# Kernel optimization log

Hardware: AMD Instinct MI355X
Metric: run time of the kernel (lower is better)

## Reference

```python
import jax, jax.numpy as jnp
import numpy as np
import math

D_MODEL = 1024
NUM_HEADS = 16
D_KEY = D_MODEL // NUM_HEADS  # 64, used only for the softmax scale
B, S = 4, 2048


def setup_inputs() -> dict:
    key = jax.random.key(0)
    ks = jax.random.split(key, 7)
    scale = 1.0 / math.sqrt(D_MODEL)
    x = jax.random.normal(ks[0], (B, S, D_MODEL), dtype=jnp.float32)
    # torch.nn.Linear params: weight [out, in], bias [out]
    Wq = jax.random.normal(ks[1], (D_MODEL, D_MODEL), dtype=jnp.float32) * scale
    bq = jax.random.normal(ks[2], (D_MODEL,), dtype=jnp.float32) * scale
    Wk = jax.random.normal(ks[3], (D_MODEL, D_MODEL), dtype=jnp.float32) * scale
    bk = jax.random.normal(ks[4], (D_MODEL,), dtype=jnp.float32) * scale
    Wv = jax.random.normal(ks[5], (D_MODEL, D_MODEL), dtype=jnp.float32) * scale
    bv = jax.random.normal(ks[6], (D_MODEL,), dtype=jnp.float32) * scale
    return {"x": x, "Wq": Wq, "bq": bq, "Wk": Wk, "bk": bk, "Wv": Wv, "bv": bv}


def reference(x, Wq, bq, Wk, bk, Wv, bv):
    # Q, K, V projections (torch Linear: x @ W.T + b)
    Q = jnp.einsum('bsd,ed->bse', x, Wq) + bq  # [B,S,D]
    K = jnp.einsum('bsd,ed->bse', x, Wk) + bk
    V = jnp.einsum('bsd,ed->bse', x, Wv) + bv
    inv_sqrt_dk = 1.0 / math.sqrt(D_KEY)
    # full-width attention (no head split, as in the source forward)
    scores = jnp.einsum('bqd,bkd->bqk', Q, K) * inv_sqrt_dk  # [B,S,S]
    weights = jax.nn.softmax(scores, axis=-1)
    return jnp.einsum('bqk,bkd->bqd', weights, V)  # [B,S,D]
```

## Files before the change

kernel.cpp:

```cpp
#include <hip/hip_runtime.h>
#include <stdint.h>

#define S_LEN 2048
#define DMODEL 1024
#define NBATCH 4
#define MROWS (NBATCH * S_LEN)

typedef __bf16 bf16x8 __attribute__((ext_vector_type(8)));
typedef float f32x4 __attribute__((ext_vector_type(4)));

__device__ __forceinline__ unsigned short f2bf(float f) {
  unsigned int x = __builtin_bit_cast(unsigned int, f);
  x += 0x7FFFu + ((x >> 16) & 1u);
  return (unsigned short)(x >> 16);
}

template <int N>
__device__ __forceinline__ void waitvm() {
  static_assert(N <= 8, "vmcnt range");
  if constexpr (N < 0) {}
  else if constexpr (N == 0) asm volatile("s_waitcnt vmcnt(0)" ::: "memory");
  else if constexpr (N == 1) asm volatile("s_waitcnt vmcnt(1)" ::: "memory");
  else if constexpr (N == 2) asm volatile("s_waitcnt vmcnt(2)" ::: "memory");
  else if constexpr (N == 3) asm volatile("s_waitcnt vmcnt(3)" ::: "memory");
  else if constexpr (N == 4) asm volatile("s_waitcnt vmcnt(4)" ::: "memory");
  else if constexpr (N == 5) asm volatile("s_waitcnt vmcnt(5)" ::: "memory");
  else if constexpr (N == 6) asm volatile("s_waitcnt vmcnt(6)" ::: "memory");
  else if constexpr (N == 7) asm volatile("s_waitcnt vmcnt(7)" ::: "memory");
  else asm volatile("s_waitcnt vmcnt(8)" ::: "memory");
}
#define BARRIER() do { __builtin_amdgcn_s_barrier(); asm volatile("" ::: "memory"); } while (0)
#define LGKM0() asm volatile("s_waitcnt lgkmcnt(0)" ::: "memory")

__global__ void prep_all_kernel(const float* __restrict__ x, const float* __restrict__ Wq,
                                const float* __restrict__ Wk, const float* __restrict__ Wv,
                                const float* __restrict__ bq, const float* __restrict__ bk,
                                ushort4* __restrict__ xb, ushort4* __restrict__ Wqkb,
                                ushort4* __restrict__ Wvb, float4* __restrict__ bqk) {
  const int NX = MROWS * DMODEL / 4;
  const int NW = DMODEL * DMODEL / 4;
  int i = blockIdx.x * blockDim.x + threadIdx.x;
  float4 v;
  if (i < NX) {
    v = reinterpret_cast<const float4*>(x)[i];
    ushort4 o; o.x = f2bf(v.x); o.y = f2bf(v.y); o.z = f2bf(v.z); o.w = f2bf(v.w);
    xb[i] = o;
  } else {
    int j = i - NX;
    if (j < NW) v = reinterpret_cast<const float4*>(Wq)[j];
    else if (j < 2 * NW) v = reinterpret_cast<const float4*>(Wk)[j - NW];
    else v = reinterpret_cast<const float4*>(Wv)[j - 2 * NW];
    ushort4 o; o.x = f2bf(v.x); o.y = f2bf(v.y); o.z = f2bf(v.z); o.w = f2bf(v.w);
    if (j < 2 * NW) Wqkb[j] = o;
    else Wvb[j - 2 * NW] = o;
    if (j < 512) bqk[j] = (j < 256) ? reinterpret_cast<const float4*>(bq)[j]
                                    : reinterpret_cast<const float4*>(bk)[j - 256];
  }
}

template <int BM_, int EP, int NT>
__global__ __launch_bounds__(512, 2) void gemm8(
    const unsigned short* __restrict__ A, const unsigned short* __restrict__ Bm,
    void* __restrict__ Cp, const float* __restrict__ bias,
    int lda, int ldb, int ldc, float scale,
    long zsA, long zsB, long zsC) {
  constexpr int BN_ = 256;
  constexpr int BK = 64;
  constexpr int RA = BM_ / 128;
  constexpr int HALF_A = (BM_ / 2) * 128;
  constexpr int HALF_B = 128 * 128;
  constexpr int ATILE = BM_ * 128;
  constexpr int BTILE = BN_ * 128;
  constexpr int MREP = BM_ / 32;
  constexpr int MQ = MREP / 2;

  __shared__ alignas(16) char lds[(ATILE + BTILE) * 2];

  const int tid = threadIdx.x;
  const int l = tid & 63;
  const int w = tid >> 6;
  const int wm = w >> 2;
  const int wn = w & 3;

  const int gx = gridDim.x;
  const int nwg = gridDim.x * gridDim.y;
  int n = blockIdx.y * gx + blockIdx.x;
  int n2 = (n & 7) * (nwg >> 3) + (n >> 3);
  const int tileM = (n2 / gx) * BM_;
  const int tileN = (n2 % gx) * BN_;

  const int z = blockIdx.z;
  const unsigned short* Ab = A + (size_t)z * zsA;
  const unsigned short* Bb = Bm + (size_t)z * zsB;

  const int srow = l >> 3;
  const int scol = (((l & 7) ^ srow) * 16);

  auto stageA = [&](int buf, int t, int h) {
#pragma unroll
    for (int r = 0; r < RA; ++r) {
      int row = h * (BM_ / 2) + r * 64 + w * 8 + srow;
      const char* g = (const char*)(Ab + (size_t)(tileM + row) * lda + t * BK) + scol;
      char* d = lds + buf * (ATILE + BTILE) + h * HALF_A + r * 8192 + w * 1024;
      __builtin_amdgcn_global_load_lds(
          (const __attribute__((address_space(1))) void*)g,
          (__attribute__((address_space(3))) void*)d, 16, 0, 0);
    }
  };
  auto stageB = [&](int buf, int t, int h) {
#pragma unroll
    for (int r = 0; r < 2; ++r) {
      int row = h * 128 + r * 64 + w * 8 + srow;
      const char* g = (const char*)(Bb + (size_t)(tileN + row) * ldb + t * BK) + scol;
      char* d = lds + buf * (ATILE + BTILE) + ATILE + h * HALF_B + r * 8192 + w * 1024;
      __builtin_amdgcn_global_load_lds(
          (const __attribute__((address_space(1))) void*)g,
          (__attribute__((address_space(3))) void*)d, 16, 0, 0);
    }
  };

  f32x4 acc[MREP][4];
#pragma unroll
  for (int m = 0; m < MREP; ++m)
#pragma unroll
    for (int nn = 0; nn < 4; ++nn) acc[m][nn] = f32x4{0.f, 0.f, 0.f, 0.f};

  const int frow = l & 15;
  auto rdA = [&](int buf, int mh, int m, int kk) -> bf16x8 {
    int row = mh * (BM_ / 2) + wm * (BM_ / 4) + m * 16 + frow;
    int col = (kk * 64 + ((l >> 4) * 16)) ^ ((row & 7) << 4);
    return *reinterpret_cast<const bf16x8*>(lds + buf * (ATILE + BTILE) + row * 128 + col);
  };
  auto rdB = [&](int buf, int nh, int nn, int kk) -> bf16x8 {
    int row = nh * 128 + wn * 32 + nn * 16 + frow;
    int col = (kk * 64 + ((l >> 4) * 16)) ^ ((row & 7) << 4);
    return *reinterpret_cast<const bf16x8*>(lds + buf * (ATILE + BTILE) + ATILE + row * 128 + col);
  };

  bf16x8 avF[MQ][2];
  bf16x8 bv0[2][2], bv1[2][2];

  auto rdAfull = [&](int buf, int mh) {
#pragma unroll
    for (int m = 0; m < MQ; ++m)
#pragma unroll
      for (int kk = 0; kk < 2; ++kk) avF[m][kk] = rdA(buf, mh, m, kk);
  };
  auto rdBfull = [&](int buf, int nh, bf16x8 (&bv)[2][2]) {
#pragma unroll
    for (int nn = 0; nn < 2; ++nn)
#pragma unroll
      for (int kk = 0; kk < 2; ++kk) bv[nn][kk] = rdB(buf, nh, nn, kk);
  };
  auto mfc = [&](int mh, bf16x8 (&bv)[2][2], int nh) {
    __builtin_amdgcn_s_setprio(1);
#pragma unroll
    for (int kk = 0; kk < 2; ++kk)
#pragma unroll
      for (int m = 0; m < MQ; ++m)
#pragma unroll
        for (int nn = 0; nn < 2; ++nn)
          acc[mh * MQ + m][nh * 2 + nn] = __builtin_amdgcn_mfma_f32_16x16x32_bf16(
              avF[m][kk], bv[nn][kk], acc[mh * MQ + m][nh * 2 + nn], 0, 0, 0);
    __builtin_amdgcn_s_setprio(0);
  };
  auto mfc2 = [&](int mh) {
    __builtin_amdgcn_s_setprio(1);
#pragma unroll
    for (int kk = 0; kk < 2; ++kk)
#pragma unroll
      for (int m = 0; m < MQ; ++m) {
#pragma unroll
        for (int nn = 0; nn < 2; ++nn)
          acc[mh * MQ + m][2 + nn] = __builtin_amdgcn_mfma_f32_16x16x32_bf16(
              avF[m][kk], bv1[nn][kk], acc[mh * MQ + m][2 + nn], 0, 0, 0);
#pragma unroll
        for (int nn = 0; nn < 2; ++nn)
          acc[mh * MQ + m][nn] = __builtin_amdgcn_mfma_f32_16x16x32_bf16(
              avF[m][kk], bv0[nn][kk], acc[mh * MQ + m][nn], 0, 0, 0);
      }
    __builtin_amdgcn_s_setprio(0);
  };

  stageA(0, 0, 0);
  stageB(0, 0, 0);
  stageB(0, 0, 1);
  stageA(0, 0, 1);
  waitvm<0>();
  BARRIER();

#pragma unroll 2
  for (int t = 0; t < NT - 1; ++t) {
    const int buf = t & 1, nb = buf ^ 1;
    rdAfull(buf, 0); rdBfull(buf, 0, bv0);
    stageA(nb, t + 1, 0); stageB(nb, t + 1, 0);
    mfc(0, bv0, 0);
    rdBfull(buf, 1, bv1);
    stageB(nb, t + 1, 1);
    mfc(0, bv1, 1);
    rdAfull(buf, 1);
    stageA(nb, t + 1, 1);
    mfc2(1);
    LGKM0();
    waitvm<0>();
    BARRIER();
  }
  {
    const int buf = (NT - 1) & 1;
    rdAfull(buf, 0); rdBfull(buf, 0, bv0);
    mfc(0, bv0, 0);
    rdBfull(buf, 1, bv1);
    mfc(0, bv1, 1);
    rdAfull(buf, 1);
    mfc2(1);
  }

  const int lr = (l >> 4) * 4;
  const int lc = l & 15;
#pragma unroll
  for (int mh = 0; mh < 2; ++mh) {
#pragma unroll
    for (int m = 0; m < MQ; ++m) {
#pragma unroll
      for (int nh = 0; nh < 2; ++nh) {
#pragma unroll
        for (int nn = 0; nn < 2; ++nn) {
          int gr = tileM + mh * (BM_ / 2) + wm * (BM_ / 4) + m * 16 + lr;
          int gc = tileN + nh * 128 + wn * 32 + nn * 16 + lc;
          f32x4 v = acc[mh * MQ + m][nh * 2 + nn];
          if constexpr (EP == 0 || EP == 3) {
            unsigned short* C = (unsigned short*)Cp + (size_t)z * zsC;
#pragma unroll
            for (int j = 0; j < 4; ++j) {
              float bb = (EP == 0) ? bias[gc] : bias[gr + j];
              C[(size_t)(gr + j) * ldc + gc] = f2bf(v[j] + bb);
            }
          } else {
            float* C = (float*)Cp + (size_t)z * zsC;
#pragma unroll
            for (int j = 0; j < 4; ++j)
              C[(size_t)(gr + j) * ldc + gc] = (EP == 1) ? v[j] * scale : v[j];
          }
        }
      }
    }
  }
}

__global__ __launch_bounds__(256) void softmax_kernel(const float* __restrict__ Sb,
                                                      unsigned short* __restrict__ P) {
  const size_t row = blockIdx.x;
  const float* sp = Sb + row * S_LEN;
  const int t = threadIdx.x;
  const int wid = t >> 6, lane = t & 63;
  float4 v0 = reinterpret_cast<const float4*>(sp)[t * 2];
  float4 v1 = reinterpret_cast<const float4*>(sp)[t * 2 + 1];
  float s[8] = {v0.x, v0.y, v0.z, v0.w, v1.x, v1.y, v1.z, v1.w};
  float mx = s[0];
#pragma unroll
  for (int i = 1; i < 8; ++i) mx = fmaxf(mx, s[i]);
#pragma unroll
  for (int o = 32; o > 0; o >>= 1) mx = fmaxf(mx, __shfl_xor(mx, o));
  __shared__ float redm[4];
  __shared__ float reds[4];
  if (lane == 0) redm[wid] = mx;
  __syncthreads();
  mx = fmaxf(fmaxf(redm[0], redm[1]), fmaxf(redm[2], redm[3]));
  float e[8];
  float sum = 0.f;
#pragma unroll
  for (int i = 0; i < 8; ++i) { e[i] = __expf(s[i] - mx); sum += e[i]; }
#pragma unroll
  for (int o = 32; o > 0; o >>= 1) sum += __shfl_xor(sum, o);
  if (lane == 0) reds[wid] = sum;
  __syncthreads();
  sum = reds[0] + reds[1] + reds[2] + reds[3];
  float inv = 1.0f / sum;
  ushort4 o0, o1;
  o0.x = f2bf(e[0] * inv); o0.y = f2bf(e[1] * inv); o0.z = f2bf(e[2] * inv); o0.w = f2bf(e[3] * inv);
  o1.x = f2bf(e[4] * inv); o1.y = f2bf(e[5] * inv); o1.z = f2bf(e[6] * inv); o1.w = f2bf(e[7] * inv);
  ushort4* dp = reinterpret_cast<ushort4*>(P + row * S_LEN);
  dp[t * 2] = o0;
  dp[t * 2 + 1] = o1;
}

extern "C" void kernel_launch(void* const* d_in, const int* in_sizes, int n_in,
                              void* d_out, int out_size, void* d_ws, size_t ws_size,
                              hipStream_t stream) {
  (void)in_sizes; (void)n_in; (void)out_size;
  const float* x = (const float*)d_in[0];
  const float* Wq = (const float*)d_in[1];
  const float* bq = (const float*)d_in[2];
  const float* Wk = (const float*)d_in[3];
  const float* bk = (const float*)d_in[4];
  const float* Wv = (const float*)d_in[5];
  const float* bv = (const float*)d_in[6];
  float* out = (float*)d_out;

  if (ws_size < 141557760ull) return;
  char* ws = (char*)d_ws;
  unsigned short* xb   = (unsigned short*)(ws);
  unsigned short* Wqkb = (unsigned short*)(ws + 16777216);
  unsigned short* Wvb  = (unsigned short*)(ws + 20971520);
  float*          bqk  = (float*)(ws + 23068672);
  unsigned short* QKb  = (unsigned short*)(ws + 24117248);
  float*          Sb   = (float*)(ws + 57671680);
  unsigned short* Vt   = (unsigned short*)(ws + 124780544);
  unsigned short* P    = QKb;

  const int NX = MROWS * DMODEL / 4, NW = DMODEL * DMODEL / 4;
  prep_all_kernel<<<dim3((NX + 3 * NW) / 256), 256, 0, stream>>>(
      x, Wq, Wk, Wv, bq, bk, (ushort4*)xb, (ushort4*)Wqkb, (ushort4*)Wvb, (float4*)bqk);

  gemm8<256, 0, 16><<<dim3(8, 32, 1), 512, 0, stream>>>(
      xb, Wqkb, QKb, bqk, 1024, 1024, 2048, 1.f, 0, 0, 0);

  gemm8<128, 3, 16><<<dim3(8, 8, 4), 512, 0, stream>>>(
      Wvb, xb, Vt, bv, 1024, 1024, 2048, 1.f,
      0, (long)S_LEN * DMODEL, (long)DMODEL * S_LEN);

  gemm8<256, 1, 16><<<dim3(8, 8, 4), 512, 0, stream>>>(
      QKb, QKb + 1024, Sb, nullptr, 2048, 2048, 2048, 0.125f,
      (long)S_LEN * 2048, (long)S_LEN * 2048, (long)S_LEN * S_LEN);

  softmax_kernel<<<dim3(MROWS), 256, 0, stream>>>(Sb, P);

  gemm8<128, 2, 32><<<dim3(4, 16, 4), 512, 0, stream>>>(
      P, Vt, out, nullptr, 2048, 2048, 1024, 1.f,
      (long)S_LEN * S_LEN, (long)DMODEL * S_LEN, (long)S_LEN * DMODEL);
}
```

Measured before the change: 169.2 us.

## Switch GEMM to triple-buffered LDS pipeline with fixed 128-row tiles

The GEMM kernel now uses three LDS buffers and prefetches two k-tiles ahead, waiting with a partial vmcnt instead of draining all loads each iteration. This is meant to hide global-to-LDS latency behind the MFMA work. The M tile is fixed at 128 rows for all GEMMs, so the QK projection and score GEMMs launch twice as many workgroups with smaller tiles. The change uses more LDS per block (3x48KB), which may limit occupancy at two blocks per CU, and lowers data reuse for the GEMMs that previously used 256-row tiles.

```diff
diff --git a/kernel.cpp b/kernel.cpp
--- a/kernel.cpp
+++ b/kernel.cpp
@@ -58,23 +58,23 @@
   }
 }
 
-template <int BM_, int EP, int NT>
+template <int EP, int NT>
 __global__ __launch_bounds__(512, 2) void gemm8(
     const unsigned short* __restrict__ A, const unsigned short* __restrict__ Bm,
     void* __restrict__ Cp, const float* __restrict__ bias,
     int lda, int ldb, int ldc, float scale,
     long zsA, long zsB, long zsC) {
+  constexpr int BM_ = 128;
   constexpr int BN_ = 256;
   constexpr int BK = 64;
-  constexpr int RA = BM_ / 128;
-  constexpr int HALF_A = (BM_ / 2) * 128;
+  constexpr int HALF_A = 64 * 128;
   constexpr int HALF_B = 128 * 128;
   constexpr int ATILE = BM_ * 128;
   constexpr int BTILE = BN_ * 128;
-  constexpr int MREP = BM_ / 32;
-  constexpr int MQ = MREP / 2;
-
-  __shared__ alignas(16) char lds[(ATILE + BTILE) * 2];
+  constexpr int BUF = ATILE + BTILE;
+  constexpr int MQ = 2;
+
+  __shared__ alignas(16) char lds[BUF * 3];
 
   const int tid = threadIdx.x;
   const int l = tid & 63;
@@ -97,44 +97,47 @@
   const int scol = (((l & 7) ^ srow) * 16);
 
   auto stageA = [&](int buf, int t, int h) {
-#pragma unroll
-    for (int r = 0; r < RA; ++r) {
-      int row = h * (BM_ / 2) + r * 64 + w * 8 + srow;
-      const char* g = (const char*)(Ab + (size_t)(tileM + row) * lda + t * BK) + scol;
-      char* d = lds + buf * (ATILE + BTILE) + h * HALF_A + r * 8192 + w * 1024;
+    int row = h * 64 + w * 8 + srow;
+    const char* g = (const char*)(Ab + (size_t)(tileM + row) * lda + t * BK) + scol;
+    char* d = lds + buf * BUF + h * HALF_A + w * 1024;
+    __builtin_amdgcn_global_load_lds(
+        (const __attribute__((address_space(1))) void*)g,
+        (__attribute__((address_space(3))) void*)d, 16, 0, 0);
+  };
+  auto stageB = [&](int buf, int t, int h) {
+#pragma unroll
+    for (int r = 0; r < 2; ++r) {
+      int row = h * 128 + r * 64 + w * 8 + srow;
+      const char* g = (const char*)(Bb + (size_t)(tileN + row) * ldb + t * BK) + scol;
+      char* d = lds + buf * BUF + ATILE + h * HALF_B + r * 8192 + w * 1024;
       __builtin_amdgcn_global_load_lds(
           (const __attribute__((address_space(1))) void*)g,
           (__attribute__((address_space(3))) void*)d, 16, 0, 0);
     }
   };
-  auto stageB = [&](int buf, int t, int h) {
-#pragma unroll
-    for (int r = 0; r < 2; ++r) {
-      int row = h * 128 + r * 64 + w * 8 + srow;
-      const char* g = (const char*)(Bb + (size_t)(tileN + row) * ldb + t * BK) + scol;
-      char* d = lds + buf * (ATILE + BTILE) + ATILE + h * HALF_B + r * 8192 + w * 1024;
-      __builtin_amdgcn_global_load_lds(
-          (const __attribute__((address_space(1))) void*)g,
-          (__attribute__((address_space(3))) void*)d, 16, 0, 0);
-    }
-  };
-
-  f32x4 acc[MREP][4];
-#pragma unroll
-  for (int m = 0; m < MREP; ++m)
+  auto stageT = [&](int buf, int t) {
+    stageA(buf, t, 0);
+    stageB(buf, t, 0);
+    stageB(buf, t, 1);
+    stageA(buf, t, 1);
+  };
+
+  f32x4 acc[4][4];
+#pragma unroll
+  for (int m = 0; m < 4; ++m)
 #pragma unroll
     for (int nn = 0; nn < 4; ++nn) acc[m][nn] = f32x4{0.f, 0.f, 0.f, 0.f};
 
   const int frow = l & 15;
   auto rdA = [&](int buf, int mh, int m, int kk) -> bf16x8 {
-    int row = mh * (BM_ / 2) + wm * (BM_ / 4) + m * 16 + frow;
+    int row = mh * 64 + wm * 32 + m * 16 + frow;
     int col = (kk * 64 + ((l >> 4) * 16)) ^ ((row & 7) << 4);
-    return *reinterpret_cast<const bf16x8*>(lds + buf * (ATILE + BTILE) + row * 128 + col);
+    return *reinterpret_cast<const bf16x8*>(lds + buf * BUF + row * 128 + col);
   };
   auto rdB = [&](int buf, int nh, int nn, int kk) -> bf16x8 {
     int row = nh * 128 + wn * 32 + nn * 16 + frow;
     int col = (kk * 64 + ((l >> 4) * 16)) ^ ((row & 7) << 4);
-    return *reinterpret_cast<const bf16x8*>(lds + buf * (ATILE + BTILE) + ATILE + row * 128 + col);
+    return *reinterpret_cast<const bf16x8*>(lds + buf * BUF + ATILE + row * 128 + col);
   };
 
   bf16x8 avF[MQ][2];
@@ -182,37 +185,37 @@
     __builtin_amdgcn_s_setprio(0);
   };
 
-  stageA(0, 0, 0);
-  stageB(0, 0, 0);
-  stageB(0, 0, 1);
-  stageA(0, 0, 1);
-  waitvm<0>();
-  BARRIER();
-
-#pragma unroll 2
-  for (int t = 0; t < NT - 1; ++t) {
-    const int buf = t & 1, nb = buf ^ 1;
-    rdAfull(buf, 0); rdBfull(buf, 0, bv0);
-    stageA(nb, t + 1, 0); stageB(nb, t + 1, 0);
-    mfc(0, bv0, 0);
-    rdBfull(buf, 1, bv1);
-    stageB(nb, t + 1, 1);
-    mfc(0, bv1, 1);
-    rdAfull(buf, 1);
-    stageA(nb, t + 1, 1);
-    mfc2(1);
-    LGKM0();
-    waitvm<0>();
-    BARRIER();
-  }
-  {
-    const int buf = (NT - 1) & 1;
+  auto tile_reads_mfma = [&](int buf) {
     rdAfull(buf, 0); rdBfull(buf, 0, bv0);
     mfc(0, bv0, 0);
     rdBfull(buf, 1, bv1);
     mfc(0, bv1, 1);
     rdAfull(buf, 1);
     mfc2(1);
+  };
+
+  stageT(0, 0);
+  stageT(1, 1);
+  waitvm<6>();
+  BARRIER();
+
+#pragma unroll 3
+  for (int t = 0; t < NT - 2; ++t) {
+    const int buf = t % 3;
+    stageT((t + 2) % 3, t + 2);
+    tile_reads_mfma(buf);
+    LGKM0();
+    waitvm<6>();
+    BARRIER();
+  }
+  {
+    tile_reads_mfma((NT - 2) % 3);
+    LGKM0();
+    waitvm<0>();
+    BARRIER();
+  }
+  {
+    tile_reads_mfma((NT - 1) % 3);
   }
 
   const int lr = (l >> 4) * 4;
@@ -225,7 +228,7 @@
       for (int nh = 0; nh < 2; ++nh) {
 #pragma unroll
         for (int nn = 0; nn < 2; ++nn) {
-          int gr = tileM + mh * (BM_ / 2) + wm * (BM_ / 4) + m * 16 + lr;
+          int gr = tileM + mh * 64 + wm * 32 + m * 16 + lr;
           int gc = tileN + nh * 128 + wn * 32 + nn * 16 + lc;
           f32x4 v = acc[mh * MQ + m][nh * 2 + nn];
           if constexpr (EP == 0 || EP == 3) {
@@ -312,20 +315,20 @@
   prep_all_kernel<<<dim3((NX + 3 * NW) / 256), 256, 0, stream>>>(
       x, Wq, Wk, Wv, bq, bk, (ushort4*)xb, (ushort4*)Wqkb, (ushort4*)Wvb, (float4*)bqk);
 
-  gemm8<256, 0, 16><<<dim3(8, 32, 1), 512, 0, stream>>>(
+  gemm8<0, 16><<<dim3(8, 64, 1), 512, 0, stream>>>(
       xb, Wqkb, QKb, bqk, 1024, 1024, 2048, 1.f, 0, 0, 0);
 
-  gemm8<128, 3, 16><<<dim3(8, 8, 4), 512, 0, stream>>>(
+  gemm8<3, 16><<<dim3(8, 8, 4), 512, 0, stream>>>(
       Wvb, xb, Vt, bv, 1024, 1024, 2048, 1.f,
       0, (long)S_LEN * DMODEL, (long)DMODEL * S_LEN);
 
-  gemm8<256, 1, 16><<<dim3(8, 8, 4), 512, 0, stream>>>(
+  gemm8<1, 16><<<dim3(8, 16, 4), 512, 0, stream>>>(
       QKb, QKb + 1024, Sb, nullptr, 2048, 2048, 2048, 0.125f,
       (long)S_LEN * 2048, (long)S_LEN * 2048, (long)S_LEN * S_LEN);
 
   softmax_kernel<<<dim3(MROWS), 256, 0, stream>>>(Sb, P);
 
-  gemm8<128, 2, 32><<<dim3(4, 16, 4), 512, 0, stream>>>(
+  gemm8<2, 32><<<dim3(4, 16, 4), 512, 0, stream>>>(
       P, Vt, out, nullptr, 2048, 2048, 1024, 1.f,
       (long)S_LEN * S_LEN, (long)DMODEL * S_LEN, (long)S_LEN * DMODEL);
 }
```

After: 178.9 us. 5.8% more time.

## Restructure GEMM main loop into barrier-separated phases with finer-grained prefetch staging

Applied to the files above, without the earlier changes.

Rewrites the double-buffered GEMM mainloop so the global-to-LDS prefetch for tile t+2 is split into quarter-tile pieces issued between MFMA phases. Each phase is fenced by barriers and explicit lgkm/vmcnt waits, which allows partial vmcnt waits instead of draining all loads each iteration. The prologue preloads nearly two stages and the last two iterations are peeled. This is meant to overlap memory traffic with MFMA work more evenly, at the cost of many extra workgroup barriers and sched_barrier fences that constrain the compiler's scheduling.

```diff
diff --git a/kernel.cpp b/kernel.cpp
--- a/kernel.cpp
+++ b/kernel.cpp
@@ -30,7 +30,8 @@
   else asm volatile("s_waitcnt vmcnt(8)" ::: "memory");
 }
 #define BARRIER() do { __builtin_amdgcn_s_barrier(); asm volatile("" ::: "memory"); } while (0)
-#define LGKM0() asm volatile("s_waitcnt lgkmcnt(0)" ::: "memory")
+#define LGKM0() do { asm volatile("s_waitcnt lgkmcnt(0)" ::: "memory"); \
+                     __builtin_amdgcn_sched_barrier(0); } while (0)
 
 __global__ void prep_all_kernel(const float* __restrict__ x, const float* __restrict__ Wq,
                                 const float* __restrict__ Wk, const float* __restrict__ Wv,
@@ -71,10 +72,11 @@
   constexpr int HALF_B = 128 * 128;
   constexpr int ATILE = BM_ * 128;
   constexpr int BTILE = BN_ * 128;
-  constexpr int MREP = BM_ / 32;
-  constexpr int MQ = MREP / 2;
-
-  __shared__ alignas(16) char lds[(ATILE + BTILE) * 2];
+  constexpr int BUF = ATILE + BTILE;
+  constexpr int MQ = BM_ / 64;
+  constexpr int VM = (BM_ == 256) ? 6 : 4;
+
+  __shared__ alignas(16) char lds[BUF * 2];
 
   const int tid = threadIdx.x;
   const int l = tid & 63;
@@ -101,7 +103,7 @@
     for (int r = 0; r < RA; ++r) {
       int row = h * (BM_ / 2) + r * 64 + w * 8 + srow;
       const char* g = (const char*)(Ab + (size_t)(tileM + row) * lda + t * BK) + scol;
-      char* d = lds + buf * (ATILE + BTILE) + h * HALF_A + r * 8192 + w * 1024;
+      char* d = lds + buf * BUF + h * HALF_A + r * 8192 + w * 1024;
       __builtin_amdgcn_global_load_lds(
           (const __attribute__((address_space(1))) void*)g,
           (__attribute__((address_space(3))) void*)d, 16, 0, 0);
@@ -112,16 +114,16 @@
     for (int r = 0; r < 2; ++r) {
       int row = h * 128 + r * 64 + w * 8 + srow;
       const char* g = (const char*)(Bb + (size_t)(tileN + row) * ldb + t * BK) + scol;
-      char* d = lds + buf * (ATILE + BTILE) + ATILE + h * HALF_B + r * 8192 + w * 1024;
+      char* d = lds + buf * BUF + ATILE + h * HALF_B + r * 8192 + w * 1024;
       __builtin_amdgcn_global_load_lds(
           (const __attribute__((address_space(1))) void*)g,
           (__attribute__((address_space(3))) void*)d, 16, 0, 0);
     }
   };
 
-  f32x4 acc[MREP][4];
-#pragma unroll
-  for (int m = 0; m < MREP; ++m)
+  f32x4 acc[2 * MQ][4];
+#pragma unroll
+  for (int m = 0; m < 2 * MQ; ++m)
 #pragma unroll
     for (int nn = 0; nn < 4; ++nn) acc[m][nn] = f32x4{0.f, 0.f, 0.f, 0.f};
 
@@ -129,12 +131,12 @@
   auto rdA = [&](int buf, int mh, int m, int kk) -> bf16x8 {
     int row = mh * (BM_ / 2) + wm * (BM_ / 4) + m * 16 + frow;
     int col = (kk * 64 + ((l >> 4) * 16)) ^ ((row & 7) << 4);
-    return *reinterpret_cast<const bf16x8*>(lds + buf * (ATILE + BTILE) + row * 128 + col);
+    return *reinterpret_cast<const bf16x8*>(lds + buf * BUF + row * 128 + col);
   };
   auto rdB = [&](int buf, int nh, int nn, int kk) -> bf16x8 {
     int row = nh * 128 + wn * 32 + nn * 16 + frow;
     int col = (kk * 64 + ((l >> 4) * 16)) ^ ((row & 7) << 4);
-    return *reinterpret_cast<const bf16x8*>(lds + buf * (ATILE + BTILE) + ATILE + row * 128 + col);
+    return *reinterpret_cast<const bf16x8*>(lds + buf * BUF + ATILE + row * 128 + col);
   };
 
   bf16x8 avF[MQ][2];
@@ -164,55 +166,70 @@
               avF[m][kk], bv[nn][kk], acc[mh * MQ + m][nh * 2 + nn], 0, 0, 0);
     __builtin_amdgcn_s_setprio(0);
   };
-  auto mfc2 = [&](int mh) {
-    __builtin_amdgcn_s_setprio(1);
-#pragma unroll
-    for (int kk = 0; kk < 2; ++kk)
-#pragma unroll
-      for (int m = 0; m < MQ; ++m) {
-#pragma unroll
-        for (int nn = 0; nn < 2; ++nn)
-          acc[mh * MQ + m][2 + nn] = __builtin_amdgcn_mfma_f32_16x16x32_bf16(
-              avF[m][kk], bv1[nn][kk], acc[mh * MQ + m][2 + nn], 0, 0, 0);
-#pragma unroll
-        for (int nn = 0; nn < 2; ++nn)
-          acc[mh * MQ + m][nn] = __builtin_amdgcn_mfma_f32_16x16x32_bf16(
-              avF[m][kk], bv0[nn][kk], acc[mh * MQ + m][nn], 0, 0, 0);
-      }
-    __builtin_amdgcn_s_setprio(0);
-  };
-
-  stageA(0, 0, 0);
-  stageB(0, 0, 0);
-  stageB(0, 0, 1);
-  stageA(0, 0, 1);
-  waitvm<0>();
+
+  stageA(0, 0, 0); stageB(0, 0, 0); stageA(0, 0, 1); stageB(0, 0, 1);
+  stageA(1, 1, 0); stageB(1, 1, 0); stageA(1, 1, 1);
+  waitvm<VM>();
   BARRIER();
 
 #pragma unroll 2
-  for (int t = 0; t < NT - 1; ++t) {
+  for (int t = 0; t < NT - 2; ++t) {
     const int buf = t & 1, nb = buf ^ 1;
     rdAfull(buf, 0); rdBfull(buf, 0, bv0);
-    stageA(nb, t + 1, 0); stageB(nb, t + 1, 0);
+    stageB(nb, t + 1, 1);
+    if constexpr (BM_ == 256) asm volatile("s_waitcnt lgkmcnt(8)" ::: "memory");
+    BARRIER(); LGKM0();
     mfc(0, bv0, 0);
+    BARRIER();
     rdBfull(buf, 1, bv1);
+    stageA(buf, t + 2, 0);
+    BARRIER(); LGKM0();
+    mfc(0, bv1, 1);
+    BARRIER();
+    rdAfull(buf, 1);
+    stageB(buf, t + 2, 0);
+    BARRIER(); LGKM0();
+    mfc(1, bv1, 1);
+    BARRIER();
+    stageA(buf, t + 2, 1);
+    waitvm<VM>();
+    BARRIER();
+    mfc(1, bv0, 0);
+    BARRIER();
+  }
+  {
+    const int t = NT - 2, buf = t & 1, nb = buf ^ 1;
+    rdAfull(buf, 0); rdBfull(buf, 0, bv0);
     stageB(nb, t + 1, 1);
+    if constexpr (BM_ == 256) asm volatile("s_waitcnt lgkmcnt(8)" ::: "memory");
+    BARRIER(); LGKM0();
+    mfc(0, bv0, 0);
+    BARRIER();
+    rdBfull(buf, 1, bv1);
+    BARRIER(); LGKM0();
     mfc(0, bv1, 1);
+    BARRIER();
     rdAfull(buf, 1);
-    stageA(nb, t + 1, 1);
-    mfc2(1);
-    LGKM0();
+    BARRIER(); LGKM0();
+    mfc(1, bv1, 1);
+    BARRIER();
     waitvm<0>();
+    BARRIER();
+    mfc(1, bv0, 0);
     BARRIER();
   }
   {
     const int buf = (NT - 1) & 1;
     rdAfull(buf, 0); rdBfull(buf, 0, bv0);
+    LGKM0();
     mfc(0, bv0, 0);
     rdBfull(buf, 1, bv1);
+    LGKM0();
     mfc(0, bv1, 1);
     rdAfull(buf, 1);
-    mfc2(1);
+    LGKM0();
+    mfc(1, bv1, 1);
+    mfc(1, bv0, 0);
   }
 
   const int lr = (l >> 4) * 4;
```

After: 173.3 us. 2.4% more time.

## Fuse exp into QK^T epilogue and defer softmax normalization to PV epilogue

Applied to the files above, without the earlier changes.

The QK^T GEMM now writes exp(score*scale) straight to bf16 P instead of fp32 scores. A light rowsum kernel computes the reciprocal row sums, and the PV GEMM multiplies each output row by that reciprocal in its epilogue. This removes the fp32 score round trip and the full softmax pass, but it drops the max subtraction, so it relies on scores staying in exp range. The GEMM main loop also swaps the single end-of-iteration vmcnt(0) and barrier for partial vmcnt waits and barriers between MFMA phases, with sched barriers, to overlap loads with compute.

```diff
diff --git a/kernel.cpp b/kernel.cpp
--- a/kernel.cpp
+++ b/kernel.cpp
@@ -30,7 +30,8 @@
   else asm volatile("s_waitcnt vmcnt(8)" ::: "memory");
 }
 #define BARRIER() do { __builtin_amdgcn_s_barrier(); asm volatile("" ::: "memory"); } while (0)
-#define LGKM0() asm volatile("s_waitcnt lgkmcnt(0)" ::: "memory")
+#define LGKM0() do { asm volatile("s_waitcnt lgkmcnt(0)" ::: "memory"); \
+                     __builtin_amdgcn_sched_barrier(0); } while (0)
 
 __global__ void prep_all_kernel(const float* __restrict__ x, const float* __restrict__ Wq,
                                 const float* __restrict__ Wk, const float* __restrict__ Wv,
@@ -73,6 +74,11 @@
   constexpr int BTILE = BN_ * 128;
   constexpr int MREP = BM_ / 32;
   constexpr int MQ = MREP / 2;
+  constexpr int VPRO = (BM_ == 256) ? 4 : 3;
+  constexpr int W_PA = (BM_ == 256) ? 6 : 4;
+  constexpr int W_PB = (BM_ == 256) ? 6 : 5;
+  constexpr int W_PC = (BM_ == 256) ? 4 : 3;
+  constexpr int VDA  = (BM_ == 256) ? 2 : 1;
 
   __shared__ alignas(16) char lds[(ATILE + BTILE) * 2];
 
@@ -186,7 +192,7 @@
   stageB(0, 0, 0);
   stageB(0, 0, 1);
   stageA(0, 0, 1);
-  waitvm<0>();
+  waitvm<VPRO>();
   BARRIER();
 
 #pragma unroll 2
@@ -194,24 +200,27 @@
     const int buf = t & 1, nb = buf ^ 1;
     rdAfull(buf, 0); rdBfull(buf, 0, bv0);
     stageA(nb, t + 1, 0); stageB(nb, t + 1, 0);
+    waitvm<W_PA>(); BARRIER(); LGKM0();
     mfc(0, bv0, 0);
     rdBfull(buf, 1, bv1);
     stageB(nb, t + 1, 1);
+    waitvm<W_PB>(); BARRIER(); LGKM0();
     mfc(0, bv1, 1);
     rdAfull(buf, 1);
     stageA(nb, t + 1, 1);
+    waitvm<W_PC>(); BARRIER(); LGKM0();
     mfc2(1);
-    LGKM0();
-    waitvm<0>();
-    BARRIER();
   }
   {
     const int buf = (NT - 1) & 1;
     rdAfull(buf, 0); rdBfull(buf, 0, bv0);
+    waitvm<VDA>(); BARRIER(); LGKM0();
     mfc(0, bv0, 0);
     rdBfull(buf, 1, bv1);
+    waitvm<0>(); BARRIER(); LGKM0();
     mfc(0, bv1, 1);
     rdAfull(buf, 1);
+    LGKM0();
     mfc2(1);
   }
 
@@ -235,6 +244,16 @@
               float bb = (EP == 0) ? bias[gc] : bias[gr + j];
               C[(size_t)(gr + j) * ldc + gc] = f2bf(v[j] + bb);
             }
+          } else if constexpr (EP == 4) {
+            unsigned short* C = (unsigned short*)Cp + (size_t)z * zsC;
+#pragma unroll
+            for (int j = 0; j < 4; ++j)
+              C[(size_t)(gr + j) * ldc + gc] = f2bf(__expf(v[j] * scale));
+          } else if constexpr (EP == 5) {
+            float* C = (float*)Cp + (size_t)z * zsC;
+#pragma unroll
+            for (int j = 0; j < 4; ++j)
+              C[(size_t)(gr + j) * ldc + gc] = v[j] * bias[(size_t)z * S_LEN + gr + j];
           } else {
             float* C = (float*)Cp + (size_t)z * zsC;
 #pragma unroll
@@ -247,41 +266,29 @@
   }
 }
 
-__global__ __launch_bounds__(256) void softmax_kernel(const float* __restrict__ Sb,
-                                                      unsigned short* __restrict__ P) {
+__global__ __launch_bounds__(256) void rowsum_kernel(const unsigned short* __restrict__ P,
+                                                     float* __restrict__ rinv) {
   const size_t row = blockIdx.x;
-  const float* sp = Sb + row * S_LEN;
+  const ushort4* sp = reinterpret_cast<const ushort4*>(P + row * S_LEN);
   const int t = threadIdx.x;
   const int wid = t >> 6, lane = t & 63;
-  float4 v0 = reinterpret_cast<const float4*>(sp)[t * 2];
-  float4 v1 = reinterpret_cast<const float4*>(sp)[t * 2 + 1];
-  float s[8] = {v0.x, v0.y, v0.z, v0.w, v1.x, v1.y, v1.z, v1.w};
-  float mx = s[0];
-#pragma unroll
-  for (int i = 1; i < 8; ++i) mx = fmaxf(mx, s[i]);
-#pragma unroll
-  for (int o = 32; o > 0; o >>= 1) mx = fmaxf(mx, __shfl_xor(mx, o));
-  __shared__ float redm[4];
-  __shared__ float reds[4];
-  if (lane == 0) redm[wid] = mx;
+  ushort4 a = sp[t * 2];
+  ushort4 b = sp[t * 2 + 1];
+  float s = 0.f;
+  s += __builtin_bit_cast(float, (unsigned int)a.x << 16);
+  s += __builtin_bit_cast(float, (unsigned int)a.y << 16);
+  s += __builtin_bit_cast(float, (unsigned int)a.z << 16);
+  s += __builtin_bit_cast(float, (unsigned int)a.w << 16);
+  s += __builtin_bit_cast(float, (unsigned int)b.x << 16);
+  s += __builtin_bit_cast(float, (unsigned int)b.y << 16);
+  s += __builtin_bit_cast(float, (unsigned int)b.z << 16);
+  s += __builtin_bit_cast(float, (unsigned int)b.w << 16);
+#pragma unroll
+  for (int o = 32; o > 0; o >>= 1) s += __shfl_xor(s, o);
+  __shared__ float red[4];
+  if (lane == 0) red[wid] = s;
   __syncthreads();
-  mx = fmaxf(fmaxf(redm[0], redm[1]), fmaxf(redm[2], redm[3]));
-  float e[8];
-  float sum = 0.f;
-#pragma unroll
-  for (int i = 0; i < 8; ++i) { e[i] = __expf(s[i] - mx); sum += e[i]; }
-#pragma unroll
-  for (int o = 32; o > 0; o >>= 1) sum += __shfl_xor(sum, o);
-  if (lane == 0) reds[wid] = sum;
-  __syncthreads();
-  sum = reds[0] + reds[1] + reds[2] + reds[3];
-  float inv = 1.0f / sum;
-  ushort4 o0, o1;
-  o0.x = f2bf(e[0] * inv); o0.y = f2bf(e[1] * inv); o0.z = f2bf(e[2] * inv); o0.w = f2bf(e[3] * inv);
-  o1.x = f2bf(e[4] * inv); o1.y = f2bf(e[5] * inv); o1.z = f2bf(e[6] * inv); o1.w = f2bf(e[7] * inv);
-  ushort4* dp = reinterpret_cast<ushort4*>(P + row * S_LEN);
-  dp[t * 2] = o0;
-  dp[t * 2 + 1] = o1;
+  if (t == 0) rinv[row] = 1.0f / (red[0] + red[1] + red[2] + red[3]);
 }
 
 extern "C" void kernel_launch(void* const* d_in, const int* in_sizes, int n_in,
@@ -297,16 +304,16 @@
   const float* bv = (const float*)d_in[6];
   float* out = (float*)d_out;
 
-  if (ws_size < 141557760ull) return;
+  if (ws_size < 108036096ull) return;
   char* ws = (char*)d_ws;
   unsigned short* xb   = (unsigned short*)(ws);
   unsigned short* Wqkb = (unsigned short*)(ws + 16777216);
   unsigned short* Wvb  = (unsigned short*)(ws + 20971520);
   float*          bqk  = (float*)(ws + 23068672);
   unsigned short* QKb  = (unsigned short*)(ws + 24117248);
-  float*          Sb   = (float*)(ws + 57671680);
-  unsigned short* Vt   = (unsigned short*)(ws + 124780544);
-  unsigned short* P    = QKb;
+  unsigned short* P    = (unsigned short*)(ws + 57671680);
+  float*          rinv = (float*)(ws + 91226112);
+  unsigned short* Vt   = (unsigned short*)(ws + 91258880);
 
   const int NX = MROWS * DMODEL / 4, NW = DMODEL * DMODEL / 4;
   prep_all_kernel<<<dim3((NX + 3 * NW) / 256), 256, 0, stream>>>(
@@ -319,13 +326,13 @@
       Wvb, xb, Vt, bv, 1024, 1024, 2048, 1.f,
       0, (long)S_LEN * DMODEL, (long)DMODEL * S_LEN);
 
-  gemm8<256, 1, 16><<<dim3(8, 8, 4), 512, 0, stream>>>(
-      QKb, QKb + 1024, Sb, nullptr, 2048, 2048, 2048, 0.125f,
+  gemm8<256, 4, 16><<<dim3(8, 8, 4), 512, 0, stream>>>(
+      QKb, QKb + 1024, P, nullptr, 2048, 2048, 2048, 0.125f,
       (long)S_LEN * 2048, (long)S_LEN * 2048, (long)S_LEN * S_LEN);
 
-  softmax_kernel<<<dim3(MROWS), 256, 0, stream>>>(Sb, P);
-
-  gemm8<128, 2, 32><<<dim3(4, 16, 4), 512, 0, stream>>>(
-      P, Vt, out, nullptr, 2048, 2048, 1024, 1.f,
+  rowsum_kernel<<<dim3(MROWS), 256, 0, stream>>>(P, rinv);
+
+  gemm8<128, 5, 32><<<dim3(4, 16, 4), 512, 0, stream>>>(
+      P, Vt, out, rinv, 2048, 2048, 1024, 1.f,
       (long)S_LEN * S_LEN, (long)DMODEL * S_LEN, (long)S_LEN * DMODEL);
 }
```

Result: faster. 155.0 us, median of 2 (-8.4%).
